# Performance work log

Hardware: AMD Instinct MI355X
Metric: run time of the kernel (lower is better)

## Reference

```python
import jax, jax.numpy as jnp
import numpy as np

N, IN, HID, HEADS, FFN = 2048, 768, 1024, 8, 2048
NH = HID // HEADS  # 128 per-head hidden


def setup_inputs() -> dict:
    key = jax.random.key(0)
    ks = jax.random.split(key, 24)
    s = 0.02
    inp = {
        "feature": jax.random.normal(ks[0], (1, N, IN), jnp.float32),
        "adj": jax.random.bernoulli(ks[1], 0.05, (1, N, N)).astype(jnp.float32),
        "gat1_W1": jax.random.normal(ks[2], (IN, HID), jnp.float32) * s,
        "gat1_a1": jax.random.normal(ks[3], (2 * NH,), jnp.float32) * s,
        "gat1_W2": jax.random.normal(ks[4], (HID, IN), jnp.float32) * s,
        "gat1_a2": jax.random.normal(ks[5], (2 * IN,), jnp.float32) * s,
        "gat2_W1": jax.random.normal(ks[6], (IN, HID), jnp.float32) * s,
        "gat2_a1": jax.random.normal(ks[7], (2 * NH,), jnp.float32) * s,
        "gat2_W2": jax.random.normal(ks[8], (HID, IN), jnp.float32) * s,
        "gat2_a2": jax.random.normal(ks[9], (2 * IN,), jnp.float32) * s,
        "Wf": jax.random.normal(ks[10], (2 * IN, IN), jnp.float32) * s,
        "bf": jnp.zeros((IN,), jnp.float32),
        "ffn_W1": jax.random.normal(ks[11], (IN, FFN), jnp.float32) * s,
        "ffn_b1": jnp.zeros((FFN,), jnp.float32),
        "ffn_W2": jax.random.normal(ks[12], (FFN, FFN), jnp.float32) * s,
        "ffn_b2": jnp.zeros((FFN,), jnp.float32),
        "ffn_W3": jax.random.normal(ks[13], (FFN, IN), jnp.float32) * s,
        "ffn_b3": jnp.zeros((IN,), jnp.float32),
        "out_W1": jax.random.normal(ks[14], (IN, FFN), jnp.float32) * s,
        "out_b1": jnp.zeros((FFN,), jnp.float32),
        "out_W2": jax.random.normal(ks[15], (FFN, IN), jnp.float32) * s,
        "out_b2": jnp.zeros((IN,), jnp.float32),
    }
    return inp


def leaky(x, slope):
    return jnp.where(x >= 0, x, slope * x)


def gat_layer(h, adjb, W, a, heads, concat):
    # h: [N, F_in]; adjb: [N, N] bool. Scores decompose since attn weight is
    # shared across heads: e_ij = leaky(a_l . g_i + a_r . g_j).
    n = h.shape[0]
    g = (h @ W).reshape(n, heads, -1)           # [N, H, F']
    f = g.shape[-1]
    gl = jnp.einsum("nhf,f->nh", g, a[:f])
    gr = jnp.einsum("nhf,f->nh", g, a[f:])
    e = leaky(gl[:, None, :] + gr[None, :, :], 0.2)   # [N, N, H]
    e = jnp.where(adjb[:, :, None], e, jnp.float32(-1e9))
    att = jax.nn.softmax(e, axis=1)             # softmax over source j
    out = jnp.einsum("ijh,jhf->ihf", att, g)    # [N, H, F']
    return out.reshape(n, -1) if concat else out.mean(axis=1)


def gat(x, adj2d, W1, a1, W2, a2):
    adjb = adj2d != 0
    x1 = jax.nn.elu(gat_layer(x, adjb, W1, a1, HEADS, True))
    return gat_layer(x1, adjb, W2, a2, 1, False)


def reference(feature, adj, gat1_W1, gat1_a1, gat1_W2, gat1_a2,
              gat2_W1, gat2_a1, gat2_W2, gat2_a2, Wf, bf,
              ffn_W1, ffn_b1, ffn_W2, ffn_b2, ffn_W3, ffn_b3,
              out_W1, out_b1, out_W2, out_b2):
    sen_adj = adj.at[:, :, -6:].set(0.0)
    sec_adj = jnp.zeros_like(adj).at[:, :, -6:].set(adj[:, :, -6:])
    x = feature[0]                               # [N, IN]
    f_sen = gat(x, sen_adj[0], gat1_W1, gat1_a1, gat1_W2, gat1_a2) + x
    f_sec = gat(x, sec_adj[0], gat2_W1, gat2_a1, gat2_W2, gat2_a2) + x
    f = jnp.concatenate([f_sec, f_sen], axis=-1)
    f = leaky(f @ Wf + bf, 0.01)                 # fusion linear + leaky
    # ffn: MLP(layers=3, keep_last=False) -> act on every layer
    f = leaky(f @ ffn_W1 + ffn_b1, 0.01)
    f = leaky(f @ ffn_W2 + ffn_b2, 0.01)
    f = leaky(f @ ffn_W3 + ffn_b3, 0.01)
    # out_ffn: MLP(layers=2)
    o = leaky(f @ out_W1 + out_b1, 0.01)
    o = leaky(o @ out_W2 + out_b2, 0.01)
    return (o + x)[None]                         # residual, [1, N, IN]
```

## Files before the change

### kernel.cpp

```cpp
#include <hip/hip_runtime.h>
#include <hip/hip_bf16.h>
#include <cmath>

#define NN 2048
#define DIN 768
#define DHID 1024
#define NHEADS 8
#define FPRIME 128
#define DFFN 2048
#define SEN_LIM 2042
#define MAXDEG 256

using short8 = __attribute__((ext_vector_type(8))) short;
using f32x4  = __attribute__((ext_vector_type(4))) float;

#if defined(__has_builtin)
#  if __has_builtin(__builtin_amdgcn_global_load_lds)
#    define HAVE_GLL 1
#  endif
#endif
#ifndef HAVE_GLL
#  define HAVE_GLL 0
#endif

__device__ inline unsigned short f2bf(float f) {
    unsigned u = __float_as_uint(f);
    unsigned r = u + 0x7FFFu + ((u >> 16) & 1u);
    return (unsigned short)(r >> 16);
}
__device__ inline float bf2f(unsigned short h) {
    return __uint_as_float(((unsigned)h) << 16);
}
__device__ inline void store_out(float* p, float v) { *p = v; }
__device__ inline void store_out(unsigned short* p, float v) { *p = f2bf(v); }

#if HAVE_GLL
__device__ inline void gll16(const unsigned short* g, unsigned short* l) {
    __builtin_amdgcn_global_load_lds(
        (const __attribute__((address_space(1))) unsigned int*)g,
        (__attribute__((address_space(3))) unsigned int*)l, 16, 0, 0);
}
#endif

template<int S> __device__ inline void wait_vmcnt() {
    if constexpr (S == 0)      asm volatile("s_waitcnt vmcnt(0)" ::: "memory");
    else if constexpr (S == 4) asm volatile("s_waitcnt vmcnt(4)" ::: "memory");
    else if constexpr (S == 6) asm volatile("s_waitcnt vmcnt(6)" ::: "memory");
    else                       asm volatile("s_waitcnt vmcnt(8)" ::: "memory");
}

__global__ __launch_bounds__(256) void build_nbrs(
    const float* __restrict__ adj,
    unsigned short* __restrict__ sen_idx, int* __restrict__ sen_cnt,
    unsigned short* __restrict__ sec_idx, int* __restrict__ sec_cnt)
{
    const int i = blockIdx.x;
    __shared__ int c_sen, c_sec;
    if (threadIdx.x == 0) { c_sen = 0; c_sec = 0; }
    __syncthreads();
    for (int j4 = threadIdx.x; j4 < NN / 4; j4 += 256) {
        float4 v = *(const float4*)&adj[(size_t)i * NN + j4 * 4];
        float vs[4] = {v.x, v.y, v.z, v.w};
        #pragma unroll
        for (int q = 0; q < 4; ++q) {
            if (vs[q] != 0.0f) {
                int j = j4 * 4 + q;
                if (j < SEN_LIM) {
                    int p = atomicAdd(&c_sen, 1);
                    if (p < MAXDEG) sen_idx[(size_t)i * MAXDEG + p] = (unsigned short)j;
                } else {
                    int p = atomicAdd(&c_sec, 1);
                    if (p < 8) sec_idx[i * 8 + p] = (unsigned short)j;
                }
            }
        }
    }
    __syncthreads();
    if (threadIdx.x == 0) { sen_cnt[i] = min(c_sen, MAXDEG); sec_cnt[i] = min(c_sec, 8); }
}

struct TPJob { const float* s; unsigned short* d; int K, N, start, trans; };
struct TPJobs { TPJob j[11]; };

__global__ __launch_bounds__(256) void mega_tp(TPJobs jobs, int njobs)
{
    __shared__ float t[32][33];
    const int tile = blockIdx.x;
    int ji = 0;
    for (int k = 1; k < 11; ++k)
        if (k < njobs && tile >= jobs.j[k].start) ji = k;
    const TPJob jb = jobs.j[ji];
    const int lt = tile - jb.start;
    const int ntx = jb.N >> 5;
    const int bn = (lt % ntx) * 32, bk = (lt / ntx) * 32;
    const int tx = threadIdx.x & 31, ty = threadIdx.x >> 5;
    if (jb.trans) {
        #pragma unroll
        for (int r = 0; r < 4; ++r)
            t[ty + r * 8][tx] = jb.s[(size_t)(bk + ty + r * 8) * jb.N + bn + tx];
        __syncthreads();
        #pragma unroll
        for (int r = 0; r < 4; ++r) {
            int n = ty + r * 8;
            jb.d[(size_t)(bn + n) * jb.K + bk + tx] = f2bf(t[tx][n]);
        }
    } else {
        #pragma unroll
        for (int r = 0; r < 4; ++r) {
            size_t e = (size_t)(bk + ty + r * 8) * jb.N + bn + tx;
            jb.d[e] = f2bf(jb.s[e]);
        }
    }
}

template<int BM, int BN, typename OUT_T>
__global__ __launch_bounds__(256) void gemm_mfma(
    const unsigned short* __restrict__ A0, const unsigned short* __restrict__ A1,
    const unsigned short* __restrict__ BT0, const unsigned short* __restrict__ BT1,
    const float* __restrict__ bias, const float* __restrict__ resid,
    OUT_T* __restrict__ C0, OUT_T* __restrict__ C1,
    unsigned short* __restrict__ Cb0, unsigned short* __restrict__ Cb1,
    int M, int N, int K, int act)
{
    constexpr int BK = 64;
    constexpr int WR = BM / 64;
    constexpr int WC = 4 / WR;
    constexpr int NF = BN / (WC * 16);
    constexpr int ACH = BM / 32;
    constexpr int BCH = BN / 32;
    constexpr int S = ACH + BCH;
    __shared__ unsigned short Asm[2][BM * BK];
    __shared__ unsigned short Bsm[2][BN * BK];
    const int z = blockIdx.z;
    const unsigned short* A  = z ? A1  : A0;
    const unsigned short* BT = z ? BT1 : BT0;
    OUT_T* C = z ? C1 : C0;
    unsigned short* Cb = z ? Cb1 : Cb0;
    const int tid = threadIdx.x;
    const int lane = tid & 63, w = tid >> 6;
    const int wr = w / WC, wc = w % WC;
    const int bm = blockIdx.y * BM, bn = blockIdx.x * BN;

    f32x4 acc[4][NF];
    #pragma unroll
    for (int mi = 0; mi < 4; ++mi)
        #pragma unroll
        for (int ni = 0; ni < NF; ++ni)
            acc[mi][ni] = (f32x4){0.f, 0.f, 0.f, 0.f};

    const unsigned short* Abase = A + (size_t)bm * K;
    const unsigned short* Bbase = BT + (size_t)bn * K;

    auto stage = [&](int b, int k0) {
        #pragma unroll
        for (int c = 0; c < ACH; ++c) {
            int e = (tid + c * 256) * 8;
            int r = e >> 6, kk = e & 63;
            int kks = kk ^ ((r & 7) << 3);
#if HAVE_GLL
            gll16(&Abase[(size_t)r * K + k0 + kks], &Asm[b][e]);
#else
            *(short8*)&Asm[b][e] = *(const short8*)&Abase[(size_t)r * K + k0 + kks];
#endif
        }
        #pragma unroll
        for (int c = 0; c < BCH; ++c) {
            int e = (tid + c * 256) * 8;
            int r = e >> 6, kk = e & 63;
            int kks = kk ^ ((r & 7) << 3);
#if HAVE_GLL
            gll16(&Bbase[(size_t)r * K + k0 + kks], &Bsm[b][e]);
#else
            *(short8*)&Bsm[b][e] = *(const short8*)&Bbase[(size_t)r * K + k0 + kks];
#endif
        }
    };

    const int nk = K / BK;
    stage(0, 0);
    int buf = 0;
    for (int t = 0; t < nk; ++t) {
        if (t + 1 < nk) {
            stage(buf ^ 1, (t + 1) * BK);
            wait_vmcnt<S>();
        } else {
            wait_vmcnt<0>();
        }
        __builtin_amdgcn_s_barrier();
        #pragma unroll
        for (int ks = 0; ks < 2; ++ks) {
            short8 af[4], bfv[NF];
            #pragma unroll
            for (int mi = 0; mi < 4; ++mi) {
                int row = wr * 64 + mi * 16 + (lane & 15);
                int col = (ks * 32 + (lane >> 4) * 8) ^ ((row & 7) << 3);
                af[mi] = *(const short8*)&Asm[buf][row * 64 + col];
            }
            #pragma unroll
            for (int ni = 0; ni < NF; ++ni) {
                int row = wc * (BN / WC) + ni * 16 + (lane & 15);
                int col = (ks * 32 + (lane >> 4) * 8) ^ ((row & 7) << 3);
                bfv[ni] = *(const short8*)&Bsm[buf][row * 64 + col];
            }
            #pragma unroll
            for (int mi = 0; mi < 4; ++mi)
                #pragma unroll
                for (int ni = 0; ni < NF; ++ni)
                    acc[mi][ni] = __builtin_amdgcn_mfma_f32_16x16x32_bf16(
                        af[mi], bfv[ni], acc[mi][ni], 0, 0, 0);
        }
        __builtin_amdgcn_s_barrier();
        buf ^= 1;
    }

    const int rbase = bm + wr * 64;
    const int cbase = bn + wc * (BN / WC);
    #pragma unroll
    for (int mi = 0; mi < 4; ++mi)
        #pragma unroll
        for (int ni = 0; ni < NF; ++ni)
            #pragma unroll
            for (int r = 0; r < 4; ++r) {
                int grow = rbase + mi * 16 + (lane >> 4) * 4 + r;
                int gcol = cbase + ni * 16 + (lane & 15);
                float v = acc[mi][ni][r];
                if (bias)  v += bias[gcol];
                if (act)   v = (v >= 0.f) ? v : 0.01f * v;
                if (resid) v += resid[(size_t)grow * N + gcol];
                store_out(&C[(size_t)grow * N + gcol], v);
                if (Cb) Cb[(size_t)grow * N + gcol] = f2bf(v);
            }
}

__global__ __launch_bounds__(64) void glgr2(
    const unsigned short* __restrict__ gA, const unsigned short* __restrict__ gB,
    int row_stride, int F, int Hlog2, int nb_per_branch,
    const float* __restrict__ aA, const float* __restrict__ aB,
    float* __restrict__ glA, float* __restrict__ grA,
    float* __restrict__ glB, float* __restrict__ grB,
    float* __restrict__ z, int zblocks)
{
    const int bid = blockIdx.x, lane = threadIdx.x;
    if (bid < zblocks) z[bid * 64 + lane] = 0.f;
    const int br = bid >= nb_per_branch;
    const int b = br ? bid - nb_per_branch : bid;
    const int node = b >> Hlog2, h = b - ((b >> Hlog2) << Hlog2);
    const unsigned short* g = (br ? gB : gA) + (size_t)node * row_stride + h * F;
    const float* a = br ? aB : aA;
    float sl = 0.f, sr = 0.f;
    for (int f = lane; f < F; f += 64) {
        float v = bf2f(g[f]);
        sl += v * a[f];
        sr += v * a[F + f];
    }
    #pragma unroll
    for (int off = 32; off > 0; off >>= 1) {
        sl += __shfl_down(sl, off);
        sr += __shfl_down(sr, off);
    }
    if (lane == 0) {
        (br ? glB : glA)[b] = sl;
        (br ? grB : grA)[b] = sr;
    }
}

__global__ __launch_bounds__(256) void col_mean2(
    const unsigned short* __restrict__ g0, const unsigned short* __restrict__ g1,
    int C, float* __restrict__ o0, float* __restrict__ o1)
{
    const unsigned short* g = blockIdx.z ? g1 : g0;
    float* o = blockIdx.z ? o1 : o0;
    int c = blockIdx.x * 256 + threadIdx.x;
    int r0 = blockIdx.y * 128;
    float s = 0.f;
    for (int r = r0; r < r0 + 128; ++r) s += bf2f(g[(size_t)r * C + c]);
    atomicAdd(&o[c], s * (1.0f / 2048.0f));
}

template<int H, int F, typename OUT_T>
__global__ __launch_bounds__(256) void attn_agg2(
    const unsigned short* __restrict__ gb0, const unsigned short* __restrict__ gb1,
    int g_stride,
    const float* __restrict__ gl0, const float* __restrict__ gr0,
    const float* __restrict__ gl1, const float* __restrict__ gr1,
    const unsigned short* __restrict__ idx0, int is0, const int* __restrict__ cnt0,
    const unsigned short* __restrict__ idx1, int is1, const int* __restrict__ cnt1,
    const float* __restrict__ gmean0, const float* __restrict__ gmean1,
    OUT_T* __restrict__ dst0, OUT_T* __restrict__ dst1,
    int dst_stride, int co0, int co1,
    const float* __restrict__ resid, int mode)
{
    constexpr int HF = H * F;
    const int bid = blockIdx.x;
    const int br = bid >= NN;
    const int i = br ? bid - NN : bid;
    const unsigned short* gbp = br ? gb1 : gb0;
    const float* gl = br ? gl1 : gl0;
    const float* gr = br ? gr1 : gr0;
    const unsigned short* idx = br ? idx1 : idx0;
    const int is = br ? is1 : is0;
    const int* cnt = br ? cnt1 : cnt0;
    const float* gmean = br ? gmean1 : gmean0;
    OUT_T* dst = br ? dst1 : dst0;
    const int co = br ? co1 : co0;

    const int tid = threadIdx.x;
    const int lane = tid & 63, w = tid >> 6;
    const int n = cnt[i];

    if (n == 0) {
        for (int c = tid; c < HF; c += 256) {
            float v = gmean[c];
            if (mode == 0) v = (v > 0.f) ? v : expm1f(v);
            else           v += resid[(size_t)i * HF + c];
            store_out(&dst[(size_t)i * dst_stride + co + c], v);
        }
        return;
    }

    __shared__ float s_wred[4 * H];
    __shared__ float s_max[H], s_inv[H], s_glh[H];
    __shared__ float s_w[128 * H];
    __shared__ unsigned short s_j[128];

    if (tid < H) s_glh[tid] = gl[(size_t)i * H + tid];
    __syncthreads();
    float glh[H];
    #pragma unroll
    for (int h = 0; h < H; ++h) glh[h] = s_glh[h];

    const unsigned short* row_idx = idx + (size_t)i * is;

    float pmax[H];
    #pragma unroll
    for (int h = 0; h < H; ++h) pmax[h] = -1e30f;
    for (int jj = tid; jj < n; jj += 256) {
        int j = row_idx[jj];
        if (H == 8) {
            float4 ga = *(const float4*)&gr[(size_t)j * 8];
            float4 gbv = *(const float4*)&gr[(size_t)j * 8 + 4];
            float sc[8] = {ga.x, ga.y, ga.z, ga.w, gbv.x, gbv.y, gbv.z, gbv.w};
            #pragma unroll
            for (int h = 0; h < H; ++h) {
                float s = glh[h] + sc[h];
                s = (s >= 0.f) ? s : 0.2f * s;
                pmax[h] = fmaxf(pmax[h], s);
            }
        } else {
            float s = glh[0] + gr[j];
            s = (s >= 0.f) ? s : 0.2f * s;
            pmax[0] = fmaxf(pmax[0], s);
        }
    }
    #pragma unroll
    for (int h = 0; h < H; ++h)
        #pragma unroll
        for (int off = 32; off > 0; off >>= 1)
            pmax[h] = fmaxf(pmax[h], __shfl_xor(pmax[h], off));
    if (lane == 0)
        #pragma unroll
        for (int h = 0; h < H; ++h) s_wred[w * H + h] = pmax[h];
    __syncthreads();
    if (tid < H)
        s_max[tid] = fmaxf(fmaxf(s_wred[tid], s_wred[H + tid]),
                           fmaxf(s_wred[2 * H + tid], s_wred[3 * H + tid]));
    __syncthreads();
    float mx[H];
    #pragma unroll
    for (int h = 0; h < H; ++h) mx[h] = s_max[h];

    float psum[H];
    #pragma unroll
    for (int h = 0; h < H; ++h) psum[h] = 0.f;
    for (int jj = tid; jj < n; jj += 256) {
        int j = row_idx[jj];
        if (H == 8) {
            float4 ga = *(const float4*)&gr[(size_t)j * 8];
            float4 gbv = *(const float4*)&gr[(size_t)j * 8 + 4];
            float sc[8] = {ga.x, ga.y, ga.z, ga.w, gbv.x, gbv.y, gbv.z, gbv.w};
            #pragma unroll
            for (int h = 0; h < H; ++h) {
                float s = glh[h] + sc[h];
                s = (s >= 0.f) ? s : 0.2f * s;
                psum[h] += expf(s - mx[h]);
            }
        } else {
            float s = glh[0] + gr[j];
            s = (s >= 0.f) ? s : 0.2f * s;
            psum[0] += expf(s - mx[0]);
        }
    }
    #pragma unroll
    for (int h = 0; h < H; ++h)
        #pragma unroll
        for (int off = 32; off > 0; off >>= 1)
            psum[h] += __shfl_xor(psum[h], off);
    if (lane == 0)
        #pragma unroll
        for (int h = 0; h < H; ++h) s_wred[w * H + h] = psum[h];
    __syncthreads();
    if (tid < H)
        s_inv[tid] = 1.f / (s_wred[tid] + s_wred[H + tid] +
                            s_wred[2 * H + tid] + s_wred[3 * H + tid]);

    const int cb = tid * 4;
    const bool active = (cb < HF);
    const int hh = (H == 8) ? (cb >> 7) : 0;
    float a0 = 0.f, a1 = 0.f, a2 = 0.f, a3 = 0.f;

    for (int c0 = 0; c0 < n; c0 += 128) {
        int m = min(128, n - c0);
        __syncthreads();
        for (int e = tid; e < m * H; e += 256) {
            int jj = (H == 8) ? (e >> 3) : e;
            int h  = (H == 8) ? (e & 7) : 0;
            int j = row_idx[c0 + jj];
            float s = glh[h] + gr[(size_t)j * H + h];
            s = (s >= 0.f) ? s : 0.2f * s;
            s_w[jj * H + h] = expf(s - s_max[h]) * s_inv[h];
            if (h == 0) s_j[jj] = (unsigned short)j;
        }
        __syncthreads();
        if (active) {
            int jj = 0;
            for (; jj + 8 <= m; jj += 8) {
                ushort4 v[8]; float wv[8];
                #pragma unroll
                for (int u = 0; u < 8; ++u) {
                    v[u] = *(const ushort4*)&gbp[(size_t)s_j[jj + u] * g_stride + cb];
                    wv[u] = s_w[(jj + u) * H + hh];
                }
                #pragma unroll
                for (int u = 0; u < 8; ++u) {
                    a0 += wv[u] * bf2f(v[u].x);
                    a1 += wv[u] * bf2f(v[u].y);
                    a2 += wv[u] * bf2f(v[u].z);
                    a3 += wv[u] * bf2f(v[u].w);
                }
            }
            for (; jj < m; ++jj) {
                ushort4 v0 = *(const ushort4*)&gbp[(size_t)s_j[jj] * g_stride + cb];
                float w0 = s_w[jj * H + hh];
                a0 += w0 * bf2f(v0.x); a1 += w0 * bf2f(v0.y);
                a2 += w0 * bf2f(v0.z); a3 += w0 * bf2f(v0.w);
            }
        }
    }

    if (active) {
        float vv[4] = {a0, a1, a2, a3};
        #pragma unroll
        for (int q = 0; q < 4; ++q) {
            float v = vv[q];
            if (mode == 0) v = (v > 0.f) ? v : expm1f(v);
            else           v += resid[(size_t)i * HF + cb + q];
            store_out(&dst[(size_t)i * dst_stride + co + cb + q], v);
        }
    }
}

extern "C" void kernel_launch(void* const* d_in, const int* in_sizes, int n_in,
                              void* d_out, int out_size, void* d_ws, size_t ws_size,
                              hipStream_t stream)
{
    const float* feature = (const float*)d_in[0];
    const float* adj     = (const float*)d_in[1];
    const float* g1W1 = (const float*)d_in[2];
    const float* g1a1 = (const float*)d_in[3];
    const float* g1W2 = (const float*)d_in[4];
    const float* g1a2 = (const float*)d_in[5];
    const float* g2W1 = (const float*)d_in[6];
    const float* g2a1 = (const float*)d_in[7];
    const float* g2W2 = (const float*)d_in[8];
    const float* g2a2 = (const float*)d_in[9];
    const float* Wf  = (const float*)d_in[10];
    const float* bfv = (const float*)d_in[11];
    const float* fW1 = (const float*)d_in[12];
    const float* fb1 = (const float*)d_in[13];
    const float* fW2 = (const float*)d_in[14];
    const float* fb2 = (const float*)d_in[15];
    const float* fW3 = (const float*)d_in[16];
    const float* fb3 = (const float*)d_in[17];
    const float* oW1 = (const float*)d_in[18];
    const float* ob1 = (const float*)d_in[19];
    const float* oW2 = (const float*)d_in[20];
    const float* ob2 = (const float*)d_in[21];
    float* out = (float*)d_out;

    char* ws = (char*)d_ws;
    size_t off = 0;
    auto alloc = [&](size_t bytes) -> void* {
        void* p = ws + off;
        off = (off + bytes + 255) & ~(size_t)255;
        return p;
    };
    typedef unsigned short bf_t;
    int* sen_cnt = (int*)alloc((size_t)NN * 4);
    int* sec_cnt = (int*)alloc((size_t)NN * 4);
    unsigned short* sen_idx = (unsigned short*)alloc((size_t)NN * MAXDEG * 2);
    unsigned short* sec_idx = (unsigned short*)alloc((size_t)NN * 8 * 2);
    bf_t*  g1b   = (bf_t*)alloc((size_t)NN * 2048 * 2);
    float* gl1a  = (float*)alloc((size_t)NN * NHEADS * 4);
    float* gr1a  = (float*)alloc((size_t)NN * NHEADS * 4);
    float* gl1b  = (float*)alloc((size_t)NN * NHEADS * 4);
    float* gr1b  = (float*)alloc((size_t)NN * NHEADS * 4);
    bf_t*  x1a   = (bf_t*)alloc((size_t)NN * DHID * 2);
    bf_t*  x1b   = (bf_t*)alloc((size_t)NN * DHID * 2);
    bf_t*  g2aB  = (bf_t*)alloc((size_t)NN * DIN * 2);
    bf_t*  g2bB  = (bf_t*)alloc((size_t)NN * DIN * 2);
    float* gl2a  = (float*)alloc((size_t)NN * 4);
    float* gr2a  = (float*)alloc((size_t)NN * 4);
    float* gl2b  = (float*)alloc((size_t)NN * 4);
    float* gr2b  = (float*)alloc((size_t)NN * 4);
    float* gmeanL1 = (float*)alloc((size_t)2048 * 4);
    float* gmeanL2 = (float*)alloc((size_t)1536 * 4);
    bf_t*  fcat  = (bf_t*)alloc((size_t)NN * (2 * DIN) * 2);
    bf_t*  fbuf  = (bf_t*)alloc((size_t)NN * DIN * 2);
    bf_t*  tA    = (bf_t*)alloc((size_t)NN * DFFN * 2);
    bf_t*  tB    = (bf_t*)alloc((size_t)NN * DFFN * 2);
    bf_t*  featb = (bf_t*)alloc((size_t)NN * DIN * 2);
    bf_t* W1T_AB = (bf_t*)alloc((size_t)2048 * DIN * 2);
    bf_t* g1W2T = (bf_t*)alloc((size_t)DHID * DIN * 2);
    bf_t* g2W2T = (bf_t*)alloc((size_t)DHID * DIN * 2);
    bf_t* WfT   = (bf_t*)alloc((size_t)(2 * DIN) * DIN * 2);
    bf_t* fW1T  = (bf_t*)alloc((size_t)DIN * DFFN * 2);
    bf_t* fW2T  = (bf_t*)alloc((size_t)DFFN * DFFN * 2);
    bf_t* fW3T  = (bf_t*)alloc((size_t)DFFN * DIN * 2);
    bf_t* oW1T  = (bf_t*)alloc((size_t)DIN * DFFN * 2);
    bf_t* oW2T  = (bf_t*)alloc((size_t)DFFN * DIN * 2);

    build_nbrs<<<NN, 256, 0, stream>>>(adj, sen_idx, sen_cnt, sec_idx, sec_cnt);

    TPJobs jobs;
    int cur = 0, nj = 0;
    auto addjob = [&](const float* s, bf_t* d, int K, int N, int trans) {
        jobs.j[nj] = {s, d, K, N, cur, trans};
        cur += (K / 32) * (N / 32);
        ++nj;
    };
    addjob(g1W1, W1T_AB, DIN, DHID, 1);
    addjob(g2W1, W1T_AB + (size_t)1024 * DIN, DIN, DHID, 1);
    addjob(g1W2, g1W2T, DHID, DIN, 1);
    addjob(g2W2, g2W2T, DHID, DIN, 1);
    addjob(Wf, WfT, 2 * DIN, DIN, 1);
    addjob(fW1, fW1T, DIN, DFFN, 1);
    addjob(fW2, fW2T, DFFN, DFFN, 1);
    addjob(fW3, fW3T, DFFN, DIN, 1);
    addjob(oW1, oW1T, DIN, DFFN, 1);
    addjob(oW2, oW2T, DFFN, DIN, 1);
    addjob(feature, featb, NN, DIN, 0);
    mega_tp<<<cur, 256, 0, stream>>>(jobs, nj);

    gemm_mfma<64, 128, bf_t><<<dim3(2048 / 128, NN / 64, 1), 256, 0, stream>>>(
        featb, nullptr, W1T_AB, nullptr, nullptr, nullptr,
        g1b, nullptr, nullptr, nullptr, NN, 2048, DIN, 0);

    glgr2<<<2 * NN * NHEADS, 64, 0, stream>>>(
        g1b, g1b + 1024, 2048, FPRIME, 3, NN * NHEADS,
        g1a1, g2a1, gl1a, gr1a, gl1b, gr1b, gmeanL1, 32);
    col_mean2<<<dim3(2048 / 256, 16, 1), 256, 0, stream>>>(
        g1b, nullptr, 2048, gmeanL1, nullptr);
    attn_agg2<NHEADS, FPRIME, bf_t><<<2 * NN, 256, 0, stream>>>(
        g1b, g1b + 1024, 2048,
        gl1a, gr1a, gl1b, gr1b,
        sen_idx, MAXDEG, sen_cnt, sec_idx, 8, sec_cnt,
        gmeanL1, gmeanL1 + 1024,
        x1a, x1b, DHID, 0, 0, nullptr, 0);

    gemm_mfma<64, 64, bf_t><<<dim3(DIN / 64, NN / 64, 2), 256, 0, stream>>>(
        x1a, x1b, g1W2T, g2W2T, nullptr, nullptr,
        g2aB, g2bB, nullptr, nullptr, NN, DIN, DHID, 0);

    glgr2<<<2 * NN, 64, 0, stream>>>(
        g2aB, g2bB, DIN, DIN, 0, NN,
        g1a2, g2a2, gl2a, gr2a, gl2b, gr2b, gmeanL2, 24);
    col_mean2<<<dim3(DIN / 256, 16, 2), 256, 0, stream>>>(
        g2aB, g2bB, DIN, gmeanL2, gmeanL2 + DIN);
    attn_agg2<1, DIN, bf_t><<<2 * NN, 256, 0, stream>>>(
        g2aB, g2bB, DIN,
        gl2a, gr2a, gl2b, gr2b,
        sen_idx, MAXDEG, sen_cnt, sec_idx, 8, sec_cnt,
        gmeanL2, gmeanL2 + DIN,
        fcat, fcat, 2 * DIN, DIN, 0, feature, 1);

    gemm_mfma<64, 64, bf_t><<<dim3(DIN / 64, NN / 64, 1), 256, 0, stream>>>(
        fcat, nullptr, WfT, nullptr, bfv, nullptr,
        fbuf, nullptr, nullptr, nullptr, NN, DIN, 2 * DIN, 1);
    gemm_mfma<64, 128, bf_t><<<dim3(DFFN / 128, NN / 64, 1), 256, 0, stream>>>(
        fbuf, nullptr, fW1T, nullptr, fb1, nullptr,
        tA, nullptr, nullptr, nullptr, NN, DFFN, DIN, 1);
    gemm_mfma<64, 128, bf_t><<<dim3(DFFN / 128, NN / 64, 1), 256, 0, stream>>>(
        tA, nullptr, fW2T, nullptr, fb2, nullptr,
        tB, nullptr, nullptr, nullptr, NN, DFFN, DFFN, 1);
    gemm_mfma<64, 64, bf_t><<<dim3(DIN / 64, NN / 64, 1), 256, 0, stream>>>(
        tB, nullptr, fW3T, nullptr, fb3, nullptr,
        fbuf, nullptr, nullptr, nullptr, NN, DIN, DFFN, 1);
    gemm_mfma<64, 128, bf_t><<<dim3(DFFN / 128, NN / 64, 1), 256, 0, stream>>>(
        fbuf, nullptr, oW1T, nullptr, ob1, nullptr,
        tA, nullptr, nullptr, nullptr, NN, DFFN, DIN, 1);
    gemm_mfma<64, 64, float><<<dim3(DIN / 64, NN / 64, 1), 256, 0, stream>>>(
        tA, nullptr, oW2T, nullptr, ob2, feature,
        out, nullptr, nullptr, nullptr, NN, DIN, DFFN, 1);
}
```

Baseline: 441.6 us.

## Cache attention scores in LDS and single-pass aggregate in attn_agg2

The leaky-relu scores computed in the max pass are now stored in shared memory, turned into exponentials in place during the sum pass, and reused as weights in the aggregation. This removes two recomputations of the gr gathers and exps, and drops the chunked re-gather loop along with its per-chunk barriers. The aggregation loop is unrolled to 16 for the multi-head case, and the single-head layer-2 launch uses 192 threads so every thread is active across the 768 columns. It assumes the degree never exceeds MAXDEG (256), since s_raw is sized to MAXDEG.

```diff
diff --git a/kernel.cpp b/kernel.cpp
--- a/kernel.cpp
+++ b/kernel.cpp
@@ -277,8 +277,8 @@
     atomicAdd(&o[c], s * (1.0f / 2048.0f));
 }
 
-template<int H, int F, typename OUT_T>
-__global__ __launch_bounds__(256) void attn_agg2(
+template<int H, int F, int BT, typename OUT_T>
+__global__ __launch_bounds__(BT) void attn_agg2(
     const unsigned short* __restrict__ gb0, const unsigned short* __restrict__ gb1,
     int g_stride,
     const float* __restrict__ gl0, const float* __restrict__ gr0,
@@ -291,6 +291,8 @@
     const float* __restrict__ resid, int mode)
 {
     constexpr int HF = H * F;
+    constexpr int NW = BT / 64;
+    constexpr int SR = (H == 8) ? 9 : 1;
     const int bid = blockIdx.x;
     const int br = bid >= NN;
     const int i = br ? bid - NN : bid;
@@ -309,7 +311,7 @@
     const int n = cnt[i];
 
     if (n == 0) {
-        for (int c = tid; c < HF; c += 256) {
+        for (int c = tid; c < HF; c += BT) {
             float v = gmean[c];
             if (mode == 0) v = (v > 0.f) ? v : expm1f(v);
             else           v += resid[(size_t)i * HF + c];
@@ -318,10 +320,9 @@
         return;
     }
 
-    __shared__ float s_wred[4 * H];
+    __shared__ float s_raw[MAXDEG * SR];
+    __shared__ float s_wred[NW * H];
     __shared__ float s_max[H], s_inv[H], s_glh[H];
-    __shared__ float s_w[128 * H];
-    __shared__ unsigned short s_j[128];
 
     if (tid < H) s_glh[tid] = gl[(size_t)i * H + tid];
     __syncthreads();
@@ -334,7 +335,7 @@
     float pmax[H];
     #pragma unroll
     for (int h = 0; h < H; ++h) pmax[h] = -1e30f;
-    for (int jj = tid; jj < n; jj += 256) {
+    for (int jj = tid; jj < n; jj += BT) {
         int j = row_idx[jj];
         if (H == 8) {
             float4 ga = *(const float4*)&gr[(size_t)j * 8];
@@ -344,11 +345,13 @@
             for (int h = 0; h < H; ++h) {
                 float s = glh[h] + sc[h];
                 s = (s >= 0.f) ? s : 0.2f * s;
+                s_raw[jj * SR + h] = s;
                 pmax[h] = fmaxf(pmax[h], s);
             }
         } else {
             float s = glh[0] + gr[j];
             s = (s >= 0.f) ? s : 0.2f * s;
+            s_raw[jj] = s;
             pmax[0] = fmaxf(pmax[0], s);
         }
     }
@@ -361,9 +364,12 @@
         #pragma unroll
         for (int h = 0; h < H; ++h) s_wred[w * H + h] = pmax[h];
     __syncthreads();
-    if (tid < H)
-        s_max[tid] = fmaxf(fmaxf(s_wred[tid], s_wred[H + tid]),
-                           fmaxf(s_wred[2 * H + tid], s_wred[3 * H + tid]));
+    if (tid < H) {
+        float m = s_wred[tid];
+        #pragma unroll
+        for (int w2 = 1; w2 < NW; ++w2) m = fmaxf(m, s_wred[w2 * H + tid]);
+        s_max[tid] = m;
+    }
     __syncthreads();
     float mx[H];
     #pragma unroll
@@ -372,22 +378,12 @@
     float psum[H];
     #pragma unroll
     for (int h = 0; h < H; ++h) psum[h] = 0.f;
-    for (int jj = tid; jj < n; jj += 256) {
-        int j = row_idx[jj];
-        if (H == 8) {
-            float4 ga = *(const float4*)&gr[(size_t)j * 8];
-            float4 gbv = *(const float4*)&gr[(size_t)j * 8 + 4];
-            float sc[8] = {ga.x, ga.y, ga.z, ga.w, gbv.x, gbv.y, gbv.z, gbv.w};
-            #pragma unroll
-            for (int h = 0; h < H; ++h) {
-                float s = glh[h] + sc[h];
-                s = (s >= 0.f) ? s : 0.2f * s;
-                psum[h] += expf(s - mx[h]);
-            }
-        } else {
-            float s = glh[0] + gr[j];
-            s = (s >= 0.f) ? s : 0.2f * s;
-            psum[0] += expf(s - mx[0]);
+    for (int jj = tid; jj < n; jj += BT) {
+        #pragma unroll
+        for (int h = 0; h < H; ++h) {
+            float e = expf(s_raw[jj * SR + h] - mx[h]);
+            s_raw[jj * SR + h] = e;
+            psum[h] += e;
         }
     }
     #pragma unroll
@@ -399,55 +395,47 @@
         #pragma unroll
         for (int h = 0; h < H; ++h) s_wred[w * H + h] = psum[h];
     __syncthreads();
-    if (tid < H)
-        s_inv[tid] = 1.f / (s_wred[tid] + s_wred[H + tid] +
-                            s_wred[2 * H + tid] + s_wred[3 * H + tid]);
+    if (tid < H) {
+        float s = s_wred[tid];
+        #pragma unroll
+        for (int w2 = 1; w2 < NW; ++w2) s += s_wred[w2 * H + tid];
+        s_inv[tid] = 1.f / s;
+    }
+    __syncthreads();
 
     const int cb = tid * 4;
     const bool active = (cb < HF);
     const int hh = (H == 8) ? (cb >> 7) : 0;
+    const float winv = s_inv[hh];
     float a0 = 0.f, a1 = 0.f, a2 = 0.f, a3 = 0.f;
 
-    for (int c0 = 0; c0 < n; c0 += 128) {
-        int m = min(128, n - c0);
-        __syncthreads();
-        for (int e = tid; e < m * H; e += 256) {
-            int jj = (H == 8) ? (e >> 3) : e;
-            int h  = (H == 8) ? (e & 7) : 0;
-            int j = row_idx[c0 + jj];
-            float s = glh[h] + gr[(size_t)j * H + h];
-            s = (s >= 0.f) ? s : 0.2f * s;
-            s_w[jj * H + h] = expf(s - s_max[h]) * s_inv[h];
-            if (h == 0) s_j[jj] = (unsigned short)j;
-        }
-        __syncthreads();
-        if (active) {
-            int jj = 0;
-            for (; jj + 8 <= m; jj += 8) {
-                ushort4 v[8]; float wv[8];
-                #pragma unroll
-                for (int u = 0; u < 8; ++u) {
-                    v[u] = *(const ushort4*)&gbp[(size_t)s_j[jj + u] * g_stride + cb];
-                    wv[u] = s_w[(jj + u) * H + hh];
-                }
-                #pragma unroll
-                for (int u = 0; u < 8; ++u) {
-                    a0 += wv[u] * bf2f(v[u].x);
-                    a1 += wv[u] * bf2f(v[u].y);
-                    a2 += wv[u] * bf2f(v[u].z);
-                    a3 += wv[u] * bf2f(v[u].w);
-                }
-            }
-            for (; jj < m; ++jj) {
-                ushort4 v0 = *(const ushort4*)&gbp[(size_t)s_j[jj] * g_stride + cb];
-                float w0 = s_w[jj * H + hh];
-                a0 += w0 * bf2f(v0.x); a1 += w0 * bf2f(v0.y);
-                a2 += w0 * bf2f(v0.z); a3 += w0 * bf2f(v0.w);
-            }
-        }
-    }
-
     if (active) {
+        constexpr int U = (H == 8) ? 16 : 8;
+        int jj = 0;
+        for (; jj + U <= n; jj += U) {
+            ushort4 v[U]; float wv[U];
+            #pragma unroll
+            for (int u = 0; u < U; ++u) {
+                int j = row_idx[jj + u];
+                v[u] = *(const ushort4*)&gbp[(size_t)j * g_stride + cb];
+                wv[u] = s_raw[(jj + u) * SR + hh] * winv;
+            }
+            #pragma unroll
+            for (int u = 0; u < U; ++u) {
+                a0 += wv[u] * bf2f(v[u].x);
+                a1 += wv[u] * bf2f(v[u].y);
+                a2 += wv[u] * bf2f(v[u].z);
+                a3 += wv[u] * bf2f(v[u].w);
+            }
+        }
+        for (; jj < n; ++jj) {
+            int j = row_idx[jj];
+            ushort4 v0 = *(const ushort4*)&gbp[(size_t)j * g_stride + cb];
+            float w0 = s_raw[jj * SR + hh] * winv;
+            a0 += w0 * bf2f(v0.x); a1 += w0 * bf2f(v0.y);
+            a2 += w0 * bf2f(v0.z); a3 += w0 * bf2f(v0.w);
+        }
+
         float vv[4] = {a0, a1, a2, a3};
         #pragma unroll
         for (int q = 0; q < 4; ++q) {
@@ -560,7 +548,7 @@
         g1a1, g2a1, gl1a, gr1a, gl1b, gr1b, gmeanL1, 32);
     col_mean2<<<dim3(2048 / 256, 16, 1), 256, 0, stream>>>(
         g1b, nullptr, 2048, gmeanL1, nullptr);
-    attn_agg2<NHEADS, FPRIME, bf_t><<<2 * NN, 256, 0, stream>>>(
+    attn_agg2<NHEADS, FPRIME, 256, bf_t><<<2 * NN, 256, 0, stream>>>(
         g1b, g1b + 1024, 2048,
         gl1a, gr1a, gl1b, gr1b,
         sen_idx, MAXDEG, sen_cnt, sec_idx, 8, sec_cnt,
@@ -576,7 +564,7 @@
         g1a2, g2a2, gl2a, gr2a, gl2b, gr2b, gmeanL2, 24);
     col_mean2<<<dim3(DIN / 256, 16, 2), 256, 0, stream>>>(
         g2aB, g2bB, DIN, gmeanL2, gmeanL2 + DIN);
-    attn_agg2<1, DIN, bf_t><<<2 * NN, 256, 0, stream>>>(
+    attn_agg2<1, DIN, 192, bf_t><<<2 * NN, 192, 0, stream>>>(
         g2aB, g2bB, DIN,
         gl2a, gr2a, gl2b, gr2b,
         sen_idx, MAXDEG, sen_cnt, sec_idx, 8, sec_cnt,
```

After: 451.8 us. 2.3% more time.
